# Kernel tuning notes

Measured on AMD Instinct MI355X. Metric: run time of the kernel, lower is better.

Reference implementation:

```python
import jax, jax.numpy as jnp
import numpy as np

B, CIN, H, W = 2, 8, 224, 224
P, S, K, WIN = 10, 5, 7, 3      # patchsize, stride, k neighbours, window radius = 15 // stride
E, F = 8, 64                    # embedding out-channels, cnn hidden features
N1 = (H - P) // S + 1
N2 = (W - P) // S + 1
N = N1 * N2                     # patches per image (43*43 = 1849)


def _conv(x, w, b):
    y = jax.lax.conv_general_dilated(x, w, (1, 1), 'SAME',
                                     dimension_numbers=('NCHW', 'OIHW', 'NCHW'))
    return y + b[None, :, None, None]


def _cnn3(x, w1, b1, w2, b2, w3, b3):
    # conv-relu, conv-relu, conv (depth=3, bn disabled)
    h = jax.nn.relu(_conv(x, w1, b1))
    h = jax.nn.relu(_conv(h, w2, b2))
    return _conv(h, w3, b3)


def _patches(x):
    # x: [B,C,H,W] -> [B, N, C*P*P] (im2col with stride S)
    ri = jnp.arange(N1)[:, None] * S + jnp.arange(P)[None, :]   # [N1,P]
    ci = jnp.arange(N2)[:, None] * S + jnp.arange(P)[None, :]   # [N2,P]
    p = x[:, :, ri, :][..., ci]            # [B,C,N1,P,N2,P]
    p = p.transpose(0, 2, 4, 1, 3, 5)      # [B,N1,N2,C,P,P]
    return p.reshape(x.shape[0], N, -1)


def _candidates():
    q1, q2 = jnp.meshgrid(jnp.arange(N1), jnp.arange(N2), indexing='ij')
    off = jnp.arange(-WIN, WIN + 1)
    c1 = jnp.clip(q1[..., None, None] + off[:, None], 0, N1 - 1)   # [N1,N2,7,7]
    c2 = jnp.clip(q2[..., None, None] + off[None, :], 0, N2 - 1)
    return (c1 * N2 + c2).reshape(N, -1)   # [N, m], m=49


def _fold(pats, C):
    # pats: [B,N,C*P*P] -> [B,C,H,W], overlap-add then normalize by counts
    pats = pats.reshape(B, N, C, P, P).transpose(0, 2, 1, 3, 4).reshape(B, C, -1)
    rr = jnp.arange(N1)[:, None] * S + jnp.arange(P)[None, :]
    cc = jnp.arange(N2)[:, None] * S + jnp.arange(P)[None, :]
    R = jnp.broadcast_to(rr[:, None, :, None], (N1, N2, P, P)).reshape(-1)
    Cc = jnp.broadcast_to(cc[None, :, None, :], (N1, N2, P, P)).reshape(-1)
    out = jnp.zeros((B, C, H, W), pats.dtype).at[:, :, R, Cc].add(pats)
    cnt = jnp.zeros((H, W), pats.dtype).at[R, Cc].add(1.0)
    return out / jnp.maximum(cnt, 1.0)


def setup_inputs() -> dict:
    key = jax.random.key(0)
    ks = jax.random.split(key, 8)
    sd = 0.05
    d = {"x": jax.random.normal(ks[0], (B, CIN, H, W), jnp.float32)}
    # embedding cnn: CIN->F->F->E
    d["w1e"] = jax.random.normal(ks[1], (F, CIN, 3, 3), jnp.float32) * sd
    d["b1e"] = jnp.zeros((F,), jnp.float32)
    d["w2e"] = jax.random.normal(ks[2], (F, F, 3, 3), jnp.float32) * sd
    d["b2e"] = jnp.zeros((F,), jnp.float32)
    d["w3e"] = jax.random.normal(ks[3], (E, F, 3, 3), jnp.float32) * sd
    d["b3e"] = jnp.zeros((E,), jnp.float32)
    # temperature cnn: CIN->F->F->1
    d["w1t"] = jax.random.normal(ks[4], (F, CIN, 3, 3), jnp.float32) * sd
    d["b1t"] = jnp.zeros((F,), jnp.float32)
    d["w2t"] = jax.random.normal(ks[5], (F, F, 3, 3), jnp.float32) * sd
    d["b2t"] = jnp.zeros((F,), jnp.float32)
    d["w3t"] = jax.random.normal(ks[6], (1, F, 3, 3), jnp.float32) * sd
    d["b3t"] = jnp.zeros((1,), jnp.float32)
    return d


def reference(x, w1e, b1e, w2e, b2e, w3e, b3e, w1t, b1t, w2t, b2t, w3t, b3t):
    xe = _cnn3(x, w1e, b1e, w2e, b2e, w3e, b3e)           # [B,E,H,W] patch embedding
    log_temp = _cnn3(x, w1t, b1t, w2t, b2t, w3t, b3t)     # [B,1,H,W] log temperature

    pe = _patches(xe)                                     # [B,N,E*P*P]
    yp = _patches(x)                                      # [B,N,CIN*P*P]
    lt = _patches(log_temp).mean(-1)                      # [B,N] per-patch log temp
    idx = _candidates()                                   # [N,m]

    # negative squared euclidean distance, gathered at window candidates
    sq = jnp.sum(pe * pe, -1)                             # [B,N]
    G = jnp.einsum('bnd,bmd->bnm', pe, pe)                # [B,N,N] patch Gram
    Dfull = -(sq[:, :, None] + sq[:, None, :] - 2.0 * G)
    Dc = Dfull[:, jnp.arange(N)[:, None], idx]            # [B,N,m]

    self_mask = (idx == jnp.arange(N)[:, None])[None]     # exclude_self=True
    logits = Dc * jnp.exp(-lt)[..., None]                 # temperature-scaled
    logits = jnp.where(self_mask, -1e9, logits)

    # continuous (neural) k-nearest-neighbour weights
    ws, cur = [], logits
    for _ in range(K):
        w = jax.nn.softmax(cur, axis=-1)
        ws.append(w)
        cur = cur + jnp.log1p(-jnp.minimum(w, 1.0 - 1e-6))
    Wk = jnp.stack(ws, axis=-1)                           # [B,N,m,K]

    yg = yp[:, idx]                                       # [B,N,m,dy] gathered neighbour patches
    nb = jnp.einsum('bnmk,bnmd->kbnd', Wk, yg)            # [K,B,N,dy]
    vols = [_fold(nb[j], CIN) for j in range(K)]
    return jnp.concatenate([x] + vols, axis=1)            # [B,(K+1)*CIN,H,W]
```

## Files before the change

### kernel.cpp

```cpp
#include <hip/hip_runtime.h>
#include <math.h>

namespace {
constexpr int B_ = 2, CIN = 8, H_ = 224, W_ = 224;
constexpr int K_ = 7;
constexpr int F_ = 64, E_ = 8;
constexpr int N1 = 43, N2 = 43, N_ = N1 * N2;
constexpr int M_ = 49;
constexpr int D_ = 800;
constexpr int HW = H_ * W_;

constexpr size_t FHW = (size_t)B_ * F_ * HW;
constexpr size_t OFF_H1E = 0;
constexpr size_t OFF_H1T = OFF_H1E + FHW;
constexpr size_t OFF_H2E = OFF_H1T + FHW;
constexpr size_t OFF_H2T = OFF_H2E + FHW;
constexpr size_t OFF_WK  = 0;
constexpr size_t OFF_XCL = OFF_H1T;
constexpr size_t OFF_XE  = OFF_H2T + FHW;
constexpr size_t OFF_LTM = OFF_XE + (size_t)B_ * E_ * HW;
constexpr size_t OFF_PE  = OFF_LTM + (size_t)B_ * HW;
constexpr size_t OFF_LT  = OFF_PE + (size_t)B_ * N_ * D_;
constexpr size_t OFF_SQ  = OFF_LT + (size_t)B_ * N_;
constexpr int WPREP_N = 294912;
constexpr int WPREP1_N = 12288;
constexpr int WPREP3_N = 9216;
constexpr int WPREP_TOT = WPREP_N + WPREP1_N + 2 * WPREP3_N;

__device__ __forceinline__ int clampi(int v, int lo, int hi) {
  return min(max(v, lo), hi);
}

__device__ __forceinline__ int xcd_swz(int x, int nwg) {
  int xcd = x & 7, idx = x >> 3;
  int q = nwg >> 3, r = nwg & 7;
  int base = (xcd < r) ? xcd * (q + 1) : r * (q + 1) + (xcd - r) * q;
  return base + idx;
}

typedef __attribute__((ext_vector_type(8))) short short8;
typedef __attribute__((ext_vector_type(4))) float float4v;
typedef __attribute__((ext_vector_type(2))) float float2v;
typedef __attribute__((ext_vector_type(4))) unsigned short ushort4v;
}

__global__ __launch_bounds__(256) void wprep_k(
    const float* __restrict__ w_e, const float* __restrict__ w_t,
    const float* __restrict__ w1e, const float* __restrict__ w1t,
    const float* __restrict__ w3e, const float* __restrict__ w3t,
    unsigned short* __restrict__ whi, unsigned short* __restrict__ wlo,
    unsigned short* __restrict__ whi1, unsigned short* __restrict__ wlo1,
    unsigned short* __restrict__ whi3, unsigned short* __restrict__ wlo3) {
  int t = blockIdx.x * 256 + threadIdx.x;
  if (t >= WPREP_TOT) return;
  float v;
  unsigned short* dh;
  unsigned short* dl;
  int di;
  if (t < WPREP_N) {
    int j = t & 7;
    int lane = (t >> 3) & 63;
    int wv = (t >> 9) & 3;
    int t2 = t >> 11;
    int idx = t2 % 9;
    int t3 = t2 / 9;
    int kcb = t3 & 1;
    int br = t3 >> 1;
    const float* wgt = br ? w_t : w_e;
    int co = wv * 16 + (lane & 15);
    int ci = kcb * 32 + 8 * (lane >> 4) + j;
    v = wgt[((size_t)co * 64 + ci) * 9 + idx];
    dh = whi; dl = wlo; di = t;
  } else if (t < WPREP_N + WPREP1_N) {
    int t1 = t - WPREP_N;
    int j = t1 & 7;
    int lane = (t1 >> 3) & 63;
    int wv = (t1 >> 9) & 3;
    int t2 = t1 >> 11;
    int ky = t2 % 3;
    int br = t2 / 3;
    const float* wgt = br ? w1t : w1e;
    int co = wv * 16 + (lane & 15);
    int kx = lane >> 4;
    int ci = j;
    v = (kx < 3) ? wgt[(((size_t)co * 8 + ci) * 3 + ky) * 3 + kx] : 0.f;
    dh = whi1; dl = wlo1; di = t1;
  } else {
    int t3v = t - WPREP_N - WPREP1_N;
    int set = t3v / WPREP3_N;
    int rem = t3v - set * WPREP3_N;
    int j = rem & 7;
    int lane = (rem >> 3) & 63;
    int t2 = rem >> 9;
    int idx = t2 % 9;
    int kcb = t2 / 9;
    int co = lane & 15;
    int ci = kcb * 32 + 8 * (lane >> 4) + j;
    if (set == 0)
      v = (co < 8) ? w3e[((size_t)co * 64 + ci) * 9 + idx] : 0.f;
    else
      v = (co == 0) ? w3t[(size_t)ci * 9 + idx] : 0.f;
    dh = whi3; dl = wlo3; di = t3v;
  }
  unsigned u = __float_as_uint(v);
  unsigned short hi = (unsigned short)(u >> 16);
  float rem = v - __uint_as_float(u & 0xffff0000u);
  unsigned short lo = (unsigned short)(__float_as_uint(rem) >> 16);
  dh[di] = hi;
  dl[di] = lo;
}

__global__ __launch_bounds__(256) void conv1_k(
    const float* __restrict__ x,
    const unsigned short* __restrict__ whi1, const unsigned short* __restrict__ wlo1,
    const float* __restrict__ b_e, float* __restrict__ o_e,
    const float* __restrict__ b_t, float* __restrict__ o_t) {
  const int tile = blockIdx.x;
  const int b = blockIdx.z & 1;
  const int br = blockIdx.z >> 1;
  const float* bias = br ? b_t : b_e;
  float* out = br ? o_t : o_e;

  const int th0 = (tile / 14) * 16, tw0 = (tile % 14) * 16;
  const int tid = threadIdx.x;
  const int wv = tid >> 6, lane = tid & 63;
  const int q = lane >> 4, n = lane & 15;

  __shared__ unsigned short sT[342 * 20];

  const float* xB = x + (size_t)b * CIN * HW;
#pragma unroll
  for (int it = 0; it < 2; ++it) {
    int s = tid + 256 * it;
    if (s < 342) {
      int lr = s / 19, lc = s - lr * 19;
      int gh = th0 + lr - 1, gw = tw0 + lc - 1;
      short8 h8, l8;
#pragma unroll
      for (int ci = 0; ci < 8; ++ci) { h8[ci] = 0; l8[ci] = 0; }
      if (lc < 18 && gh >= 0 && gh < H_ && gw >= 0 && gw < W_) {
        const float* xp = xB + (size_t)gh * W_ + gw;
#pragma unroll
        for (int ci = 0; ci < 8; ++ci) {
          float v = xp[(size_t)ci * HW];
          unsigned u = __float_as_uint(v);
          float rem = v - __uint_as_float(u & 0xffff0000u);
          h8[ci] = (short)(u >> 16);
          l8[ci] = (short)(__float_as_uint(rem) >> 16);
        }
      }
      *(short8*)&sT[s * 20] = h8;
      *(short8*)&sT[s * 20 + 8] = l8;
    }
  }

  const short8* wh8 = (const short8*)whi1;
  const short8* wl8 = (const short8*)wlo1;
  short8 Ah[3], Al[3];
#pragma unroll
  for (int ky = 0; ky < 3; ++ky) {
    int ab = ((br * 3 + ky) * 4 + wv) * 64 + lane;
    Ah[ky] = wh8[ab];
    Al[ky] = wl8[ab];
  }

  float4v acc[16];
#pragma unroll
  for (int pr = 0; pr < 16; ++pr) acc[pr] = (float4v)0.f;

  __syncthreads();

#pragma unroll
  for (int r = 0; r < 18; ++r) {
    const unsigned short* p = &sT[(r * 19 + n + q) * 20];
    short8 Bh = *(const short8*)p;
    short8 Bl = *(const short8*)(p + 8);
#pragma unroll
    for (int ky = 0; ky < 3; ++ky) {
      const int pr = r - ky;
      if (pr >= 0 && pr < 16) {
        acc[pr] = __builtin_amdgcn_mfma_f32_16x16x32_bf16(Ah[ky], Bh, acc[pr], 0, 0, 0);
        acc[pr] = __builtin_amdgcn_mfma_f32_16x16x32_bf16(Al[ky], Bh, acc[pr], 0, 0, 0);
        acc[pr] = __builtin_amdgcn_mfma_f32_16x16x32_bf16(Ah[ky], Bl, acc[pr], 0, 0, 0);
      }
    }
  }

  float4v bv = *(const float4v*)&bias[wv * 16 + 4 * q];
#pragma unroll
  for (int pr = 0; pr < 16; ++pr) {
    float4v v;
#pragma unroll
    for (int r = 0; r < 4; ++r) v[r] = fmaxf(acc[pr][r] + bv[r], 0.f);
    *(float4v*)&out[(((size_t)b * H_ + th0 + pr) * W_ + tw0 + n) * 64 + wv * 16 + 4 * q] = v;
  }
}

__global__ __launch_bounds__(256) void conv2_mfma_k(
    const float* __restrict__ in_e, const float* __restrict__ in_t,
    const unsigned short* __restrict__ whi, const unsigned short* __restrict__ wlo,
    const float* __restrict__ b_e, const float* __restrict__ b_t,
    unsigned short* __restrict__ ehi, unsigned short* __restrict__ elo,
    unsigned short* __restrict__ thi, unsigned short* __restrict__ tlo) {
  constexpr int NLD = 21;
  const int tile = blockIdx.x;
  const int b = blockIdx.z & 1;
  const int br = blockIdx.z >> 1;
  const float* in = br ? in_t : in_e;
  const float* bias = br ? b_t : b_e;
  unsigned short* ohi = br ? thi : ehi;
  unsigned short* olo = br ? tlo : elo;

  const int th0 = (tile / 14) * 16, tw0 = (tile % 14) * 16;
  const int tid = threadIdx.x;
  const int wv = tid >> 6, lane = tid & 63;
  const int q = lane >> 4, n = lane & 15;

  __shared__ unsigned short sT[18 * 18 * 72];
  unsigned* sT32 = (unsigned*)sT;

  float4v acc[16];
#pragma unroll
  for (int pr = 0; pr < 16; ++pr) acc[pr] = (float4v)0.f;

  const float* inB = in + (size_t)b * HW * 64;
  const short8* whi8 = (const short8*)whi;
  const short8* wlo8 = (const short8*)wlo;

  int po[NLD];
  unsigned okm = 0;
#pragma unroll
  for (int j = 0; j < NLD; ++j) {
    int s = tid + 256 * j;
    int sp = s >> 4, cp = s & 15;
    int lr = sp / 18, lc = sp - lr * 18;
    int gh = th0 + lr - 1, gw = tw0 + lc - 1;
    bool ok = (s < 5184) && gh >= 0 && gh < H_ && gw >= 0 && gw < W_;
    po[j] = ok ? (gh * W_ + gw) * 64 + 2 * cp : 0;
    if (ok) okm |= (1u << j);
  }

  for (int kcb = 0; kcb < 2; ++kcb) {
    float2 stg[NLD];
#pragma unroll
    for (int j = 0; j < NLD; ++j)
      stg[j] = *(const float2*)&inB[(size_t)po[j] + kcb * 32];

    __syncthreads();
#pragma unroll
    for (int j = 0; j < NLD; ++j) {
      int s = tid + 256 * j;
      if (s < 5184) {
        int sp = s >> 4, cp = s & 15;
        bool ok = (okm >> j) & 1;
        float vx = ok ? stg[j].x : 0.f;
        float vy = ok ? stg[j].y : 0.f;
        unsigned u0 = __float_as_uint(vx), u1 = __float_as_uint(vy);
        float r0 = vx - __uint_as_float(u0 & 0xffff0000u);
        float r1 = vy - __uint_as_float(u1 & 0xffff0000u);
        unsigned l0 = __float_as_uint(r0) >> 16, l1 = __float_as_uint(r1) >> 16;
        sT32[sp * 36 + cp] = (u0 >> 16) | ((u1 >> 16) << 16);
        sT32[sp * 36 + 16 + cp] = l0 | (l1 << 16);
      }
    }
    __syncthreads();

    short8 Ah[9], Al[9];
    const int abase = (((br * 2 + kcb) * 9) * 4 + wv) * 64 + lane;
#pragma unroll
    for (int idx = 0; idx < 9; ++idx) {
      Ah[idx] = whi8[abase + idx * 256];
      Al[idx] = wlo8[abase + idx * 256];
    }

#pragma unroll
    for (int r = 0; r < 18; ++r) {
      short8 Bh[3], Bl[3];
#pragma unroll
      for (int kx = 0; kx < 3; ++kx) {
        const unsigned short* p = &sT[(r * 18 + n + kx) * 72 + 8 * q];
        Bh[kx] = *(const short8*)p;
        Bl[kx] = *(const short8*)(p + 32);
      }
#pragma unroll
      for (int ky = 0; ky < 3; ++ky) {
        const int pr = r - ky;
        if (pr >= 0 && pr < 16) {
#pragma unroll
          for (int kx = 0; kx < 3; ++kx) {
            const int idx = ky * 3 + kx;
            acc[pr] = __builtin_amdgcn_mfma_f32_16x16x32_bf16(Ah[idx], Bh[kx], acc[pr], 0, 0, 0);
            acc[pr] = __builtin_amdgcn_mfma_f32_16x16x32_bf16(Al[idx], Bh[kx], acc[pr], 0, 0, 0);
            acc[pr] = __builtin_amdgcn_mfma_f32_16x16x32_bf16(Ah[idx], Bl[kx], acc[pr], 0, 0, 0);
          }
        }
      }
    }
  }

  float4v bv = *(const float4v*)&bias[wv * 16 + 4 * q];
  unsigned short* sHi = (unsigned short*)sT;
  unsigned short* sLo = sHi + 128 * 68;
  __syncthreads();
#pragma unroll
  for (int hf = 0; hf < 2; ++hf) {
#pragma unroll
    for (int pr8 = 0; pr8 < 8; ++pr8) {
      int pr = hf * 8 + pr8;
      int px = pr8 * 16 + n;
      ushort4v hv, lv;
#pragma unroll
      for (int r = 0; r < 4; ++r) {
        float v = fmaxf(acc[pr][r] + bv[r], 0.f);
        unsigned u = __float_as_uint(v);
        float rem = v - __uint_as_float(u & 0xffff0000u);
        hv[r] = (unsigned short)(u >> 16);
        lv[r] = (unsigned short)(__float_as_uint(rem) >> 16);
      }
      *(ushort4v*)&sHi[px * 68 + wv * 16 + 4 * q] = hv;
      *(ushort4v*)&sLo[px * 68 + wv * 16 + 4 * q] = lv;
    }
    __syncthreads();
#pragma unroll
    for (int i = 0; i < 4; ++i) {
      int f = tid + 256 * i;
      int px = f >> 3, c8 = f & 7;
      int h = th0 + hf * 8 + (px >> 4), w = tw0 + (px & 15);
      size_t o = ((size_t)(b * H_ + h) * W_ + w) * 64 + c8 * 8;
      *(short8*)&ohi[o] = *(const short8*)&sHi[px * 68 + c8 * 8];
      *(short8*)&olo[o] = *(const short8*)&sLo[px * 68 + c8 * 8];
    }
    __syncthreads();
  }
}

__global__ __launch_bounds__(256) void conv3_mfma_k(
    const unsigned short* __restrict__ h2ehi, const unsigned short* __restrict__ h2elo,
    const unsigned short* __restrict__ h2thi, const unsigned short* __restrict__ h2tlo,
    const unsigned short* __restrict__ whi3, const unsigned short* __restrict__ wlo3,
    const float* __restrict__ b3e, const float* __restrict__ b3t,
    float* __restrict__ xe, float* __restrict__ ltm) {
  constexpr int NLD = 12;
  const int tile = blockIdx.x;
  const int b = blockIdx.z & 1;
  const int br = blockIdx.z >> 1;
  const unsigned short* ihi = (br ? h2thi : h2ehi) + (size_t)b * HW * 64;
  const unsigned short* ilo = (br ? h2tlo : h2elo) + (size_t)b * HW * 64;

  const int th0 = (tile / 14) * 8, tw0 = (tile % 14) * 16;
  const int tid = threadIdx.x;
  const int wv = tid >> 6, lane = tid & 63;
  const int q = lane >> 4, n = lane & 15;

  __shared__ unsigned short sT[180 * 72];
  unsigned* sT32 = (unsigned*)sT;

  int po[NLD];
  unsigned okm = 0;
#pragma unroll
  for (int j = 0; j < NLD; ++j) {
    int s = tid + 256 * j;
    int sp = s >> 4, cp = s & 15;
    int lr = sp / 18, lc = sp - lr * 18;
    int gh = th0 + lr - 1, gw = tw0 + lc - 1;
    bool ok = (s < 2880) && gh >= 0 && gh < H_ && gw >= 0 && gw < W_;
    po[j] = ok ? (gh * W_ + gw) * 64 + 2 * cp : 0;
    if (ok) okm |= (1u << j);
  }

  const short8* wh8 = (const short8*)whi3;
  const short8* wl8 = (const short8*)wlo3;
  const int brBase = br * 1152;

  float4v acc[2];
  acc[0] = (float4v)0.f;
  acc[1] = (float4v)0.f;

  for (int kcb = 0; kcb < 2; ++kcb) {
    unsigned sgh[NLD], sgl[NLD];
#pragma unroll
    for (int j = 0; j < NLD; ++j) {
      sgh[j] = *(const unsigned*)&ihi[(size_t)po[j] + kcb * 32];
      sgl[j] = *(const unsigned*)&ilo[(size_t)po[j] + kcb * 32];
    }
    __syncthreads();
#pragma unroll
    for (int j = 0; j < NLD; ++j) {
      int s = tid + 256 * j;
      if (s < 2880) {
        int sp = s >> 4, cp = s & 15;
        bool ok = (okm >> j) & 1;
        sT32[sp * 36 + cp] = ok ? sgh[j] : 0u;
        sT32[sp * 36 + 16 + cp] = ok ? sgl[j] : 0u;
      }
    }
    __syncthreads();

    short8 Ah[9], Al[9];
#pragma unroll
    for (int idx = 0; idx < 9; ++idx) {
      int fe = brBase + (kcb * 9 + idx) * 64 + lane;
      Ah[idx] = wh8[fe];
      Al[idx] = wl8[fe];
    }

#pragma unroll
    for (int r = 0; r < 4; ++r) {
      const int rr = 2 * wv + r;
      short8 Bh[3], Bl[3];
#pragma unroll
      for (int kx = 0; kx < 3; ++kx) {
        const unsigned short* p = &sT[(rr * 18 + n + kx) * 72 + 8 * q];
        Bh[kx] = *(const short8*)p;
        Bl[kx] = *(const short8*)(p + 32);
      }
#pragma unroll
      for (int ky = 0; ky < 3; ++ky) {
        const int pl = r - ky;
        if (pl >= 0 && pl < 2) {
#pragma unroll
          for (int kx = 0; kx < 3; ++kx) {
            const int idx = ky * 3 + kx;
            acc[pl] = __builtin_amdgcn_mfma_f32_16x16x32_bf16(Ah[idx], Bh[kx], acc[pl], 0, 0, 0);
            acc[pl] = __builtin_amdgcn_mfma_f32_16x16x32_bf16(Al[idx], Bh[kx], acc[pl], 0, 0, 0);
            acc[pl] = __builtin_amdgcn_mfma_f32_16x16x32_bf16(Ah[idx], Bl[kx], acc[pl], 0, 0, 0);
          }
        }
      }
    }
  }

  if (br == 0) {
    if (q < 2) {
      float4v bv = *(const float4v*)&b3e[4 * q];
#pragma unroll
      for (int pl = 0; pl < 2; ++pl) {
        int h = th0 + 2 * wv + pl;
#pragma unroll
        for (int r = 0; r < 4; ++r)
          xe[((size_t)(b * 8 + 4 * q + r) * H_ + h) * W_ + tw0 + n] = acc[pl][r] + bv[r];
      }
    }
  } else {
    if (q == 0) {
      float bt = b3t[0];
#pragma unroll
      for (int pl = 0; pl < 2; ++pl) {
        int h = th0 + 2 * wv + pl;
        ltm[(size_t)b * HW + h * W_ + tw0 + n] = acc[pl][0] + bt;
      }
    }
  }
}

__global__ __launch_bounds__(256) void xcl_k(const float* __restrict__ x,
                                             float* __restrict__ xcl) {
  int i = blockIdx.x * 256 + threadIdx.x;
  if (i >= B_ * HW) return;
  int b = i / HW, pix = i % HW;
  const float* xp = x + (size_t)b * CIN * HW + pix;
  float4v v0, v1;
#pragma unroll
  for (int c = 0; c < 4; ++c) v0[c] = xp[(size_t)c * HW];
#pragma unroll
  for (int c = 0; c < 4; ++c) v1[c] = xp[(size_t)(4 + c) * HW];
  *(float4v*)&xcl[(size_t)i * 8] = v0;
  *(float4v*)&xcl[(size_t)i * 8 + 4] = v1;
}

__global__ __launch_bounds__(256) void prep_k(const float* __restrict__ xe,
                                              const float* __restrict__ ltm,
                                              float* __restrict__ pe,
                                              float* __restrict__ lt,
                                              float* __restrict__ sq) {
  const int n = blockIdx.x, b = blockIdx.y;
  const int tid = threadIdx.x;
  const int wv = tid >> 6, lane = tid & 63;
  const int q1 = n / N2, q2 = n % N2;
  const int r0 = q1 * 5, c0 = q2 * 5;

  float s = 0.f;
  float* peR = pe + ((size_t)b * N_ + n) * D_;
#pragma unroll
  for (int j = 0; j < 4; ++j) {
    int d = tid + 256 * j;
    if (d < D_) {
      int c = d / 100;
      int rr = (d / 10) % 10;
      int cc = d % 10;
      size_t si = ((size_t)(b * 8 + c) * H_ + r0 + rr) * W_ + c0 + cc;
      float ve = xe[si];
      peR[d] = ve;
      s += ve * ve;
    }
  }
  float t = 0.f;
  if (tid < 100) t = ltm[(size_t)b * HW + (r0 + tid / 10) * W_ + c0 + tid % 10];

#pragma unroll
  for (int off = 32; off > 0; off >>= 1) {
    s += __shfl_xor(s, off);
    t += __shfl_xor(t, off);
  }
  __shared__ float rs[4], rt[4];
  if (lane == 0) { rs[wv] = s; rt[wv] = t; }
  __syncthreads();
  if (tid == 0) {
    sq[b * N_ + n] = rs[0] + rs[1] + rs[2] + rs[3];
    lt[b * N_ + n] = (rt[0] + rt[1] + rt[2] + rt[3]) * 0.01f;
  }
}

__global__ __launch_bounds__(256) void attn_w_k(const float* __restrict__ pe,
                                                const float* __restrict__ lt,
                                                const float* __restrict__ sq,
                                                float* __restrict__ wk) {
  const int wv = threadIdx.x >> 6, lane = threadIdx.x & 63;
  const int ng = xcd_swz(blockIdx.x, (N_ + 3) / 4);
  const int n = ng * 4 + wv;
  if (n >= N_) return;
  const int b = blockIdx.y;
  const int q1 = n / N2, q2 = n % N2;

  const float* peB = pe + (size_t)b * N_ * D_;
  const float* qrow = peB + (size_t)n * D_;
  float q[13];
#pragma unroll
  for (int t = 0; t < 13; ++t) {
    int s = t * 64 + lane;
    q[t] = (s < D_) ? qrow[s] : 0.f;
  }

  const float sqn = sq[b * N_ + n];
  const float itemp = expf(-lt[b * N_ + n]);
  float gm = -INFINITY;

  for (int o1 = 0; o1 < 7; ++o1) {
    int c1 = clampi(q1 + o1 - 3, 0, N1 - 1);
    const float* rowb = peB + (size_t)(c1 * N2) * D_;
#pragma unroll
    for (int o2 = 0; o2 < 7; ++o2) {
      int c2 = clampi(q2 + o2 - 3, 0, N2 - 1);
      int cn = c1 * N2 + c2;
      const float* crow = rowb + (size_t)c2 * D_;
      float a = 0.f;
#pragma unroll
      for (int t = 0; t < 13; ++t) {
        float v;
        if (t < 12) v = crow[t * 64 + lane];
        else v = (lane < 32) ? crow[768 + lane] : 0.f;
        a += q[t] * v;
      }
#pragma unroll
      for (int off = 32; off > 0; off >>= 1) a += __shfl_xor(a, off);
      float Dv = -(sqn + sq[b * N_ + cn] - 2.f * a);
      float lg = (cn == n) ? -1e9f : Dv * itemp;
      const int m = o1 * 7 + o2;
      gm = (lane == m) ? lg : gm;
    }
  }

  float cur = (lane < M_) ? gm : -INFINITY;
  float* wrow = wk + (size_t)(b * N_ + n) * (M_ * K_);
#pragma unroll
  for (int k = 0; k < K_; ++k) {
    float mx = cur;
#pragma unroll
    for (int off = 32; off > 0; off >>= 1) mx = fmaxf(mx, __shfl_xor(mx, off));
    float e = (lane < M_) ? expf(cur - mx) : 0.f;
    float ssum = e;
#pragma unroll
    for (int off = 32; off > 0; off >>= 1) ssum += __shfl_xor(ssum, off);
    float w = e / ssum;
    if (lane < M_) wrow[lane * K_ + k] = w;
    cur += log1pf(-fminf(w, 1.f - 1e-6f));
  }
}

__global__ __launch_bounds__(256) void foldpv_k(const float* __restrict__ xcl,
                                                const float* __restrict__ wk,
                                                float* __restrict__ out) {
  const int tile = xcd_swz(blockIdx.x, 196);
  const int b = blockIdx.y;
  const int c0 = blockIdx.z * 4;
  const int ty0 = (tile / 14) * 16, tx0 = (tile % 14) * 16;
  const int tid = threadIdx.x;
  const int h = ty0 + (tid >> 4), w = tx0 + (tid & 15);

  const int q1lo_t = max(0, (ty0 - 5) / 5), q1hi_t = min(N1 - 1, (ty0 + 15) / 5);
  const int q2lo_t = max(0, (tx0 - 5) / 5), q2hi_t = min(N2 - 1, (tx0 + 15) / 5);
  const int nq1 = q1hi_t - q1lo_t + 1, nq2 = q2hi_t - q2lo_t + 1;

  __shared__ float sWk[25 * 392];
  {
    const int tot = nq1 * nq2 * 392;
    for (int s = tid; s < tot; s += 256) {
      int lq = s / 392, r = s - lq * 392;
      int m = r >> 3, k = r & 7;
      int n = (q1lo_t + lq / nq2) * N2 + (q2lo_t + lq % nq2);
      sWk[s] = (k < 7) ? wk[(size_t)(b * N_ + n) * (M_ * K_) + m * 7 + k] : 0.f;
    }
  }
  __syncthreads();

  const float* xclB = xcl + (size_t)b * HW * 8;
  const int pix = h * W_ + w;
  float* outB = out + (size_t)b * 64 * HW + pix;

  {
    float4v pv = *(const float4v*)&xclB[(size_t)pix * 8 + c0];
#pragma unroll
    for (int c = 0; c < 4; ++c) outB[(size_t)(c0 + c) * HW] = pv[c];
  }

  const int q1lo = max(0, (h - 5) / 5), q1hi = min(N1 - 1, h / 5);
  const int q2lo = max(0, (w - 5) / 5), q2hi = min(N2 - 1, w / 5);

  float acc[4][7];
#pragma unroll
  for (int c = 0; c < 4; ++c)
#pragma unroll
    for (int k = 0; k < 7; ++k) acc[c][k] = 0.f;

  int cnt = 0;
  for (int q1 = q1lo; q1 <= q1hi; ++q1) {
    const int ib = h - 5 * q1;
    const int lq1 = q1 - q1lo_t;
    for (int q2 = q2lo; q2 <= q2hi; ++q2) {
      ++cnt;
      const int jb = w - 5 * q2;
      const float* wq = sWk + (lq1 * nq2 + (q2 - q2lo_t)) * 392;
#pragma unroll
      for (int o1 = 0; o1 < 7; ++o1) {
        const int c1 = clampi(q1 + o1 - 3, 0, N1 - 1);
        const int row = c1 * 5 + ib;
#pragma unroll
        for (int o2 = 0; o2 < 7; ++o2) {
          const int c2 = clampi(q2 + o2 - 3, 0, N2 - 1);
          const int col = c2 * 5 + jb;
          float4v xv = *(const float4v*)&xclB[((size_t)row * W_ + col) * 8 + c0];
          const float* wp = wq + (o1 * 7 + o2) * 8;
          float4v w4 = *(const float4v*)wp;
          float2v w2 = *(const float2v*)(wp + 4);
          float w6 = wp[6];
#pragma unroll
          for (int c = 0; c < 4; ++c) {
            acc[c][0] += w4[0] * xv[c];
            acc[c][1] += w4[1] * xv[c];
            acc[c][2] += w4[2] * xv[c];
            acc[c][3] += w4[3] * xv[c];
            acc[c][4] += w2[0] * xv[c];
            acc[c][5] += w2[1] * xv[c];
            acc[c][6] += w6 * xv[c];
          }
        }
      }
    }
  }

  const float inv = (cnt > 0) ? 1.f / (float)cnt : 0.f;
#pragma unroll
  for (int k = 0; k < 7; ++k)
#pragma unroll
    for (int c = 0; c < 4; ++c)
      outB[(size_t)(8 + k * 8 + c0 + c) * HW] = acc[c][k] * inv;
}

extern "C" void kernel_launch(void* const* d_in, const int* in_sizes, int n_in,
                              void* d_out, int out_size, void* d_ws,
                              size_t ws_size, hipStream_t stream) {
  const float* x   = (const float*)d_in[0];
  const float* w1e = (const float*)d_in[1];
  const float* b1e = (const float*)d_in[2];
  const float* w2e = (const float*)d_in[3];
  const float* b2e = (const float*)d_in[4];
  const float* w3e = (const float*)d_in[5];
  const float* b3e = (const float*)d_in[6];
  const float* w1t = (const float*)d_in[7];
  const float* b1t = (const float*)d_in[8];
  const float* w2t = (const float*)d_in[9];
  const float* b2t = (const float*)d_in[10];
  const float* w3t = (const float*)d_in[11];
  const float* b3t = (const float*)d_in[12];

  float* ws  = (float*)d_ws;
  float* out = (float*)d_out;

  float* h1e = ws + OFF_H1E;
  float* h1t = ws + OFF_H1T;
  unsigned short* h2ehi = (unsigned short*)(ws + OFF_H2E);
  unsigned short* h2elo = h2ehi + (size_t)B_ * HW * 64;
  unsigned short* h2thi = (unsigned short*)(ws + OFF_H2T);
  unsigned short* h2tlo = h2thi + (size_t)B_ * HW * 64;
  float* wkb = ws + OFF_WK;
  float* xe  = ws + OFF_XE;
  float* ltm = ws + OFF_LTM;
  float* pe  = ws + OFF_PE;
  float* lt  = ws + OFF_LT;
  float* sqv = ws + OFF_SQ;
  unsigned short* whi  = (unsigned short*)(ws + OFF_XE);
  unsigned short* wlo  = whi + WPREP_N;
  unsigned short* whi1 = wlo + WPREP_N;
  unsigned short* wlo1 = whi1 + WPREP1_N;
  unsigned short* whi3 = (unsigned short*)(ws + OFF_PE);
  unsigned short* wlo3 = whi3 + 2 * WPREP3_N;
  float* xcl = ws + OFF_XCL;

  wprep_k<<<(WPREP_TOT + 255) / 256, 256, 0, stream>>>(
      w2e, w2t, w1e, w1t, w3e, w3t, whi, wlo, whi1, wlo1, whi3, wlo3);
  conv1_k<<<dim3(196, 1, 4), 256, 0, stream>>>(x, whi1, wlo1, b1e, h1e, b1t, h1t);
  conv2_mfma_k<<<dim3(196, 1, 4), 256, 0, stream>>>(h1e, h1t, whi, wlo, b2e, b2t,
                                                    h2ehi, h2elo, h2thi, h2tlo);
  xcl_k<<<(B_ * HW + 255) / 256, 256, 0, stream>>>(x, xcl);
  conv3_mfma_k<<<dim3(392, 1, 4), 256, 0, stream>>>(h2ehi, h2elo, h2thi, h2tlo,
                                                    whi3, wlo3, b3e, b3t, xe, ltm);
  prep_k<<<dim3(N_, B_), 256, 0, stream>>>(xe, ltm, pe, lt, sqv);
  attn_w_k<<<dim3((N_ + 3) / 4, B_), 256, 0, stream>>>(pe, lt, sqv, wkb);
  foldpv_k<<<dim3(196, B_, 2), 256, 0, stream>>>(xcl, wkb, out);
}
```

Baseline: 301.4 us.

## Add interior fast path to fold that pre-averages neighbour weights per cell

For interior tiles away from borders, every pixel is covered by exactly four patches, and the clamped neighbour offsets reduce to fixed pixel shifts. The fold can therefore average the four patches' weight rows once per 5x5 cell in shared memory and then do a single 49-term weighted gather per pixel. The previous code looped over four patches per pixel, each with 49 gathers. This removes roughly three quarters of the gather and FMA work on interior tiles. The cost is a second code path with divergent block behaviour and more complex staging of the weights.

After: 280.5 us. 6.9% less time.

```diff
diff --git a/kernel.cpp b/kernel.cpp
--- a/kernel.cpp
+++ b/kernel.cpp
@@ -583,44 +583,101 @@
   const int tile = xcd_swz(blockIdx.x, 196);
   const int b = blockIdx.y;
   const int c0 = blockIdx.z * 4;
-  const int ty0 = (tile / 14) * 16, tx0 = (tile % 14) * 16;
+  const int t1 = tile / 14, t2 = tile % 14;
+  const int ty0 = t1 * 16, tx0 = t2 * 16;
   const int tid = threadIdx.x;
   const int h = ty0 + (tid >> 4), w = tx0 + (tid & 15);
+  const bool fast = (t1 >= 2 && t1 <= 11 && t2 >= 2 && t2 <= 11);
+
+  __shared__ float smem[25 * 392];
+
+  const float* xclB = xcl + (size_t)b * HW * 8;
+  const int pix = h * W_ + w;
+  float* outB = out + (size_t)b * 64 * HW + pix;
+
+  {
+    float4v pv = *(const float4v*)&xclB[(size_t)pix * 8 + c0];
+#pragma unroll
+    for (int c = 0; c < 4; ++c) outB[(size_t)(c0 + c) * HW] = pv[c];
+  }
+
+  float acc[4][7];
+#pragma unroll
+  for (int c = 0; c < 4; ++c)
+#pragma unroll
+    for (int k = 0; k < 7; ++k) acc[c][k] = 0.f;
+
+  if (fast) {
+    const int cl1_0 = (ty0 - 5) / 5, cl2_0 = (tx0 - 5) / 5;
+    for (int s = tid; s < 16 * 392; s += 256) {
+      int cell = s / 392, r = s - cell * 392;
+      int m = r >> 3, k = r & 7;
+      float v = 0.f;
+      if (k < 7) {
+        int q1c = cl1_0 + (cell >> 2), q2c = cl2_0 + (cell & 3);
+        size_t base = (size_t)(b * N_ + q1c * N2 + q2c) * (M_ * K_) + m * 7 + k;
+        v = 0.25f * (wk[base] + wk[base + M_ * K_] +
+                     wk[base + (size_t)N2 * (M_ * K_)] +
+                     wk[base + (size_t)(N2 + 1) * (M_ * K_)]);
+      }
+      smem[s] = v;
+    }
+    __syncthreads();
+
+    const int cl1 = (h - 5) / 5 - cl1_0, cl2 = (w - 5) / 5 - cl2_0;
+    const float* sSp = smem + (cl1 * 4 + cl2) * 392;
+    int roff[7], coff[7];
+#pragma unroll
+    for (int o = 0; o < 7; ++o) {
+      roff[o] = (h + 5 * (o - 3)) * W_;
+      coff[o] = w + 5 * (o - 3);
+    }
+#pragma unroll
+    for (int o1 = 0; o1 < 7; ++o1) {
+#pragma unroll
+      for (int o2 = 0; o2 < 7; ++o2) {
+        float4v xv = *(const float4v*)&xclB[((size_t)(roff[o1] + coff[o2])) * 8 + c0];
+        const float* sp = sSp + (o1 * 7 + o2) * 8;
+        float4v w4 = *(const float4v*)sp;
+        float2v w2 = *(const float2v*)(sp + 4);
+        float w6 = sp[6];
+#pragma unroll
+        for (int c = 0; c < 4; ++c) {
+          acc[c][0] += w4[0] * xv[c];
+          acc[c][1] += w4[1] * xv[c];
+          acc[c][2] += w4[2] * xv[c];
+          acc[c][3] += w4[3] * xv[c];
+          acc[c][4] += w2[0] * xv[c];
+          acc[c][5] += w2[1] * xv[c];
+          acc[c][6] += w6 * xv[c];
+        }
+      }
+    }
+#pragma unroll
+    for (int k = 0; k < 7; ++k)
+#pragma unroll
+      for (int c = 0; c < 4; ++c)
+        outB[(size_t)(8 + k * 8 + c0 + c) * HW] = acc[c][k];
+    return;
+  }
 
   const int q1lo_t = max(0, (ty0 - 5) / 5), q1hi_t = min(N1 - 1, (ty0 + 15) / 5);
   const int q2lo_t = max(0, (tx0 - 5) / 5), q2hi_t = min(N2 - 1, (tx0 + 15) / 5);
   const int nq1 = q1hi_t - q1lo_t + 1, nq2 = q2hi_t - q2lo_t + 1;
 
-  __shared__ float sWk[25 * 392];
   {
     const int tot = nq1 * nq2 * 392;
     for (int s = tid; s < tot; s += 256) {
       int lq = s / 392, r = s - lq * 392;
       int m = r >> 3, k = r & 7;
       int n = (q1lo_t + lq / nq2) * N2 + (q2lo_t + lq % nq2);
-      sWk[s] = (k < 7) ? wk[(size_t)(b * N_ + n) * (M_ * K_) + m * 7 + k] : 0.f;
+      smem[s] = (k < 7) ? wk[(size_t)(b * N_ + n) * (M_ * K_) + m * 7 + k] : 0.f;
     }
   }
   __syncthreads();
-
-  const float* xclB = xcl + (size_t)b * HW * 8;
-  const int pix = h * W_ + w;
-  float* outB = out + (size_t)b * 64 * HW + pix;
-
-  {
-    float4v pv = *(const float4v*)&xclB[(size_t)pix * 8 + c0];
-#pragma unroll
-    for (int c = 0; c < 4; ++c) outB[(size_t)(c0 + c) * HW] = pv[c];
-  }
 
   const int q1lo = max(0, (h - 5) / 5), q1hi = min(N1 - 1, h / 5);
   const int q2lo = max(0, (w - 5) / 5), q2hi = min(N2 - 1, w / 5);
-
-  float acc[4][7];
-#pragma unroll
-  for (int c = 0; c < 4; ++c)
-#pragma unroll
-    for (int k = 0; k < 7; ++k) acc[c][k] = 0.f;
 
   int cnt = 0;
   for (int q1 = q1lo; q1 <= q1hi; ++q1) {
@@ -629,7 +686,7 @@
     for (int q2 = q2lo; q2 <= q2hi; ++q2) {
       ++cnt;
       const int jb = w - 5 * q2;
-      const float* wq = sWk + (lq1 * nq2 + (q2 - q2lo_t)) * 392;
+      const float* wq = smem + (lq1 * nq2 + (q2 - q2lo_t)) * 392;
 #pragma unroll
       for (int o1 = 0; o1 < 7; ++o1) {
         const int c1 = clampi(q1 + o1 - 3, 0, N1 - 1);
```
